# Optimization experiments

Hardware: AMD Instinct MI355X
Metric: run time of the kernel (lower is better)

Reference implementation:

```python
import jax, jax.numpy as jnp
import numpy as np
from jax import lax

B, T, D, NL, NH, FF, NC, SMAX, MAXS = 4, 160000, 768, 12, 12, 2048, 100, 64, 200
CONV_SPEC = [(512, 10, 5), (512, 3, 2), (512, 3, 2), (512, 3, 2), (512, 2, 2), (512, 2, 2), (768, 2, 2)]
TP = 499  # frames after conv stack for T=160000


def _ln(x, w, b, eps=1e-5):
    m = x.mean(-1, keepdims=True)
    v = ((x - m) ** 2).mean(-1, keepdims=True)
    return (x - m) * lax.rsqrt(v + eps) * w + b


def setup_inputs() -> dict:
    key = jax.random.key(0)
    ks = iter(jax.random.split(key, 64))
    d = {}
    d['x'] = jax.random.normal(next(ks), (B, 1, T), jnp.float32)
    d['seg_bounds'] = jnp.sort(jax.random.randint(next(ks), (B, SMAX + 1), 0, TP), axis=-1)
    d['n_segs'] = jax.random.randint(next(ks), (B,), SMAX // 2, SMAX + 1)
    in_c = 1
    for i, (oc, k, s) in enumerate(CONV_SPEC):
        d[f'conv_w{i}'] = jax.random.normal(next(ks), (oc, in_c, k), jnp.float32) * 0.02
        d[f'conv_b{i}'] = jnp.zeros((oc,), jnp.float32)
        in_c = oc
    d['attn_v'] = jax.random.normal(next(ks), (D,), jnp.float32)  # torch.randn init
    d['pos_emb'] = jax.random.normal(next(ks), (MAXS, D), jnp.float32) * 0.02
    d['in_w'] = jax.random.normal(next(ks), (NL, 3 * D, D), jnp.float32) * 0.02
    d['in_b'] = jnp.zeros((NL, 3 * D), jnp.float32)
    d['out_w'] = jax.random.normal(next(ks), (NL, D, D), jnp.float32) * 0.02
    d['out_b'] = jnp.zeros((NL, D), jnp.float32)
    d['ff1_w'] = jax.random.normal(next(ks), (NL, FF, D), jnp.float32) * 0.02
    d['ff1_b'] = jnp.zeros((NL, FF), jnp.float32)
    d['ff2_w'] = jax.random.normal(next(ks), (NL, D, FF), jnp.float32) * 0.02
    d['ff2_b'] = jnp.zeros((NL, D), jnp.float32)
    d['ln1_w'] = jnp.ones((NL, D), jnp.float32)
    d['ln1_b'] = jnp.zeros((NL, D), jnp.float32)
    d['ln2_w'] = jnp.ones((NL, D), jnp.float32)
    d['ln2_b'] = jnp.zeros((NL, D), jnp.float32)
    d['fln_w'] = jnp.ones((D,), jnp.float32)
    d['fln_b'] = jnp.zeros((D,), jnp.float32)
    d['proj_w'] = jax.random.normal(next(ks), (NC, D), jnp.float32) * 0.02
    d['proj_b'] = jnp.zeros((NC,), jnp.float32)
    return d


def reference(x, seg_bounds, n_segs,
              conv_w0, conv_b0, conv_w1, conv_b1, conv_w2, conv_b2, conv_w3, conv_b3,
              conv_w4, conv_b4, conv_w5, conv_b5, conv_w6, conv_b6,
              attn_v, pos_emb, in_w, in_b, out_w, out_b,
              ff1_w, ff1_b, ff2_w, ff2_b, ln1_w, ln1_b, ln2_w, ln2_b,
              fln_w, fln_b, proj_w, proj_b):
    # ---- conv feature extractor (Conv1d + ReLU stack), NCW layout ----
    ws = [conv_w0, conv_w1, conv_w2, conv_w3, conv_w4, conv_w5, conv_w6]
    bs = [conv_b0, conv_b1, conv_b2, conv_b3, conv_b4, conv_b5, conv_b6]
    h = x
    for w, b, (_, _, s) in zip(ws, bs, CONV_SPEC):
        h = lax.conv_general_dilated(h, w, (s,), 'VALID',
                                     dimension_numbers=('NCH', 'OIH', 'NCH'))
        h = jax.nn.relu(h + b[None, :, None])
    feats = h.transpose(0, 2, 1)  # [B, Tp, D]
    Tp = feats.shape[1]

    # ---- vectorized per-segment attention pooling (replaces ragged python loop) ----
    starts = jnp.clip(seg_bounds[:, :-1], 0, Tp - 1)           # [B, Smax]
    ends = jnp.maximum(starts + 1, jnp.clip(seg_bounds[:, 1:], 0, Tp))
    pad_mask = jnp.arange(SMAX)[None, :] >= n_segs[:, None]    # [B, Smax] True=pad
    t = jnp.arange(Tp)
    fm = (t[None, None, :] >= starts[..., None]) & (t[None, None, :] < ends[..., None]) \
         & (~pad_mask[..., None])                              # [B, Smax, Tp]
    scores = jnp.einsum('btc,c->bt', feats, attn_v)[:, None, :]  # [B, 1, Tp]
    m = jnp.max(jnp.where(fm, scores, -jnp.inf), axis=-1, keepdims=True)
    m = jnp.where(jnp.isfinite(m), m, 0.0)
    e = jnp.where(fm, jnp.exp(scores - m), 0.0)
    den = e.sum(-1, keepdims=True)
    wgt = e / jnp.where(den > 0, den, 1.0)                     # masked softmax over frames
    tokens = jnp.einsum('bst,btc->bsc', wgt, feats)            # [B, Smax, D]; pads are zeros

    tokens = tokens + pos_emb[:SMAX][None]

    # ---- post-norm transformer encoder (torch TransformerEncoderLayer defaults) ----
    dh = D // NH
    scale = 1.0 / np.sqrt(dh)

    def layer(tok, p):
        iw, ib, ow, ob, f1w, f1b, f2w, f2b, l1w, l1b, l2w, l2b = p
        qkv = tok @ iw.T + ib
        q, k, v = jnp.split(qkv, 3, axis=-1)
        def heads(z):
            return z.reshape(B, SMAX, NH, dh).transpose(0, 2, 1, 3)
        q, k, v = heads(q), heads(k), heads(v)
        att = jnp.einsum('bhqd,bhkd->bhqk', q, k) * scale
        att = jnp.where(pad_mask[:, None, None, :], -1e9, att)  # key padding mask
        att = jax.nn.softmax(att, axis=-1)
        o = jnp.einsum('bhqk,bhkd->bhqd', att, v).transpose(0, 2, 1, 3).reshape(B, SMAX, D)
        o = o @ ow.T + ob
        tok = _ln(tok + o, l1w, l1b)
        f = jax.nn.relu(tok @ f1w.T + f1b) @ f2w.T + f2b
        tok = _ln(tok + f, l2w, l2b)
        return tok, None

    tokens, _ = lax.scan(layer, tokens,
                         (in_w, in_b, out_w, out_b, ff1_w, ff1_b, ff2_w, ff2_b,
                          ln1_w, ln1_b, ln2_w, ln2_b))

    y = _ln(tokens, fln_w, fln_b)
    logits = y @ proj_w.T + proj_b
    return logits, pad_mask
```

## Files before the change

kernel.cpp:

```cpp
#include <hip/hip_runtime.h>
#include <hip/hip_bf16.h>

#define BATCH 4
#define TIN0 160000
#define DMODEL 768
#define NLAYER 12
#define FFDIM 2048
#define NCLS 100
#define SMAX_ 64
#define TP_ 499

typedef __attribute__((ext_vector_type(8))) short short8;
typedef __attribute__((ext_vector_type(4))) float f32x4;

__device__ inline ushort f2b(float f) { __hip_bfloat16 h = __float2bfloat16(f); return *(ushort*)&h; }
__device__ inline float b2f(ushort u) { __hip_bfloat16 h = *(__hip_bfloat16*)&u; return __bfloat162float(h); }

__device__ inline void gl_lds16(const ushort* g, ushort* l) {
    __builtin_amdgcn_global_load_lds((const __attribute__((address_space(1))) unsigned int*)g,
                                     (__attribute__((address_space(3))) unsigned int*)l, 16, 0, 0);
}

__device__ inline float wave_reduce_sum(float v) {
#pragma unroll
    for (int off = 32; off > 0; off >>= 1) v += __shfl_down(v, off, 64);
    return v;
}
__device__ inline float wave_reduce_max(float v) {
#pragma unroll
    for (int off = 32; off > 0; off >>= 1) v = fmaxf(v, __shfl_down(v, off, 64));
    return v;
}
__device__ inline float block_reduce_sum(float v, float* scratch) {
    v = wave_reduce_sum(v);
    int wid = threadIdx.x >> 6;
    if ((threadIdx.x & 63) == 0) scratch[wid] = v;
    __syncthreads();
    float r = scratch[0] + scratch[1] + scratch[2] + scratch[3];
    __syncthreads();
    return r;
}
__device__ inline float block_reduce_max(float v, float* scratch) {
    v = wave_reduce_max(v);
    int wid = threadIdx.x >> 6;
    if ((threadIdx.x & 63) == 0) scratch[wid] = v;
    __syncthreads();
    float r = fmaxf(fmaxf(scratch[0], scratch[1]), fmaxf(scratch[2], scratch[3]));
    __syncthreads();
    return r;
}

template <int KW, int STRIDE, int RELU, int OBF, int BF32>
__global__ __launch_bounds__(256) void conv_mfma(
    const ushort* __restrict__ A,
    const ushort* __restrict__ Wc,
    const float* __restrict__ Wf,
    const float* __restrict__ bias,
    void* __restrict__ outv,
    int Cin, int Cout, int Tout, int tBase, int uBase,
    long aStride, long oStride) {
    const int K = KW * Cin;
    const int nCh = K >> 5;
    const int CPK = Cin >> 5;
    const int t0 = tBase + blockIdx.x * 128;
    const int oc0 = blockIdx.y * 128;
    const int b = blockIdx.z;
    const ushort* Ab = A + (size_t)b * aStride;

    __shared__ ushort sA[4096];
    __shared__ ushort sB[4096];

    const int tid = threadIdx.x;
    const int lane = tid & 63;
    const int wv = tid >> 6;
    const int rsub = lane >> 2;
    const int kgW = (lane & 3) ^ ((lane >> 3) & 3);
    const int mrow = lane & 15;
    const int kq = lane >> 4;
    const int slot8 = (mrow * 4 + (kq ^ ((mrow >> 1) & 3))) * 8;

    f32x4 acc[2][8];
#pragma unroll
    for (int s = 0; s < 2; s++)
#pragma unroll
        for (int n = 0; n < 8; n++) acc[s][n] = (f32x4){0.f, 0.f, 0.f, 0.f};

    for (int c = 0; c < nCh; c++) {
        const int kw = (KW == 1) ? 0 : (c / CPK);
        const int icc = (c - kw * CPK) << 5;
#pragma unroll
        for (int j = 0; j < 2; j++) {
            int t = t0 + j * 64 + wv * 16 + rsub;
            if (t > Tout - 1) t = Tout - 1;
            int u = STRIDE * t + kw - uBase;
            gl_lds16(Ab + (size_t)u * Cin + icc + kgW * 8, &sA[(j * 64 + wv * 16) * 32]);
        }
#pragma unroll
        for (int j = 0; j < 2; j++) {
            int rowb = oc0 + j * 64 + wv * 16 + rsub;
            if (rowb > Cout - 1) rowb = Cout - 1;
            if (BF32) {
                const float* wp = Wf + (size_t)rowb * K + c * 32 + kgW * 8;
                float4 w0_ = *(const float4*)wp;
                float4 w1_ = *(const float4*)(wp + 4);
                short8 vals;
                vals[0] = (short)f2b(w0_.x); vals[1] = (short)f2b(w0_.y);
                vals[2] = (short)f2b(w0_.z); vals[3] = (short)f2b(w0_.w);
                vals[4] = (short)f2b(w1_.x); vals[5] = (short)f2b(w1_.y);
                vals[6] = (short)f2b(w1_.z); vals[7] = (short)f2b(w1_.w);
                *(short8*)&sB[(j * 64 + wv * 16) * 32 + lane * 8] = vals;
            } else {
                gl_lds16(Wc + (size_t)rowb * K + c * 32 + kgW * 8, &sB[(j * 64 + wv * 16) * 32]);
            }
        }
        __syncthreads();
        short8 a0 = *(const short8*)&sA[(wv * 32 + 0) * 32 + slot8];
        short8 a1 = *(const short8*)&sA[(wv * 32 + 16) * 32 + slot8];
#pragma unroll
        for (int n = 0; n < 8; n++) {
            short8 bf = *(const short8*)&sB[(n * 16) * 32 + slot8];
            acc[0][n] = __builtin_amdgcn_mfma_f32_16x16x32_bf16(a0, bf, acc[0][n], 0, 0, 0);
            acc[1][n] = __builtin_amdgcn_mfma_f32_16x16x32_bf16(a1, bf, acc[1][n], 0, 0, 0);
        }
        __syncthreads();
    }

    float* outf = (float*)outv + (size_t)b * oStride;
    ushort* outh = (ushort*)outv + (size_t)b * oStride;
    float bz[8];
#pragma unroll
    for (int n = 0; n < 8; n++) {
        int oc = oc0 + n * 16 + mrow;
        bz[n] = (oc < Cout) ? bias[oc] : 0.f;
    }
#pragma unroll
    for (int s = 0; s < 2; s++) {
        int tb = t0 + wv * 32 + s * 16 + kq * 4;
#pragma unroll
        for (int n = 0; n < 8; n++) {
            int oc = oc0 + n * 16 + mrow;
            if (oc >= Cout) continue;
#pragma unroll
            for (int r = 0; r < 4; r++) {
                int t = tb + r;
                if (t < Tout) {
                    float v = acc[s][n][r] + bz[n];
                    if (RELU) v = fmaxf(v, 0.f);
                    if (OBF) outh[(size_t)t * Cout + oc] = f2b(v);
                    else outf[(size_t)t * Cout + oc] = v;
                }
            }
        }
    }
}

__global__ __launch_bounds__(256) void gemm_sk(
    const ushort* __restrict__ A, const float* __restrict__ Wf,
    const float* __restrict__ bias, float* __restrict__ outp,
    int M, int K, int KCH, long oSlab) {
    __shared__ ushort sA[4096];
    __shared__ ushort sB[4096];
    const int tid = threadIdx.x;
    const int lane = tid & 63;
    const int wv = tid >> 6;
    const int rsub = lane >> 2;
    const int kgW = (lane & 3) ^ ((lane >> 3) & 3);
    const int mrow = lane & 15;
    const int kq = lane >> 4;
    const int slot8 = (mrow * 4 + (kq ^ ((mrow >> 1) & 3))) * 8;
    const int t0 = blockIdx.x * 128;
    const int oc0 = blockIdx.y * 128;
    const int kc = blockIdx.z;
    const int k0 = kc * KCH;

    f32x4 acc[2][8];
#pragma unroll
    for (int s = 0; s < 2; s++)
#pragma unroll
        for (int n = 0; n < 8; n++) acc[s][n] = (f32x4){0.f, 0.f, 0.f, 0.f};

    const int nIt = KCH >> 5;
    for (int c = 0; c < nIt; c++) {
        const int kk = k0 + (c << 5);
#pragma unroll
        for (int j = 0; j < 2; j++) {
            int t = t0 + j * 64 + wv * 16 + rsub;
            gl_lds16(A + (size_t)t * K + kk + kgW * 8, &sA[(j * 64 + wv * 16) * 32]);
        }
#pragma unroll
        for (int j = 0; j < 2; j++) {
            int rowb = oc0 + j * 64 + wv * 16 + rsub;
            const float* wp = Wf + (size_t)rowb * K + kk + kgW * 8;
            float4 w0_ = *(const float4*)wp;
            float4 w1_ = *(const float4*)(wp + 4);
            short8 vals;
            vals[0] = (short)f2b(w0_.x); vals[1] = (short)f2b(w0_.y);
            vals[2] = (short)f2b(w0_.z); vals[3] = (short)f2b(w0_.w);
            vals[4] = (short)f2b(w1_.x); vals[5] = (short)f2b(w1_.y);
            vals[6] = (short)f2b(w1_.z); vals[7] = (short)f2b(w1_.w);
            *(short8*)&sB[(j * 64 + wv * 16) * 32 + lane * 8] = vals;
        }
        __syncthreads();
        short8 a0 = *(const short8*)&sA[(wv * 32 + 0) * 32 + slot8];
        short8 a1 = *(const short8*)&sA[(wv * 32 + 16) * 32 + slot8];
#pragma unroll
        for (int n = 0; n < 8; n++) {
            short8 bf = *(const short8*)&sB[(n * 16) * 32 + slot8];
            acc[0][n] = __builtin_amdgcn_mfma_f32_16x16x32_bf16(a0, bf, acc[0][n], 0, 0, 0);
            acc[1][n] = __builtin_amdgcn_mfma_f32_16x16x32_bf16(a1, bf, acc[1][n], 0, 0, 0);
        }
        __syncthreads();
    }

    float* op = outp + (size_t)kc * oSlab;
#pragma unroll
    for (int s = 0; s < 2; s++) {
        int tb = t0 + wv * 32 + s * 16 + kq * 4;
#pragma unroll
        for (int n = 0; n < 8; n++) {
            int oc = oc0 + n * 16 + mrow;
            float bz = (kc == 0) ? bias[oc] : 0.f;
#pragma unroll
            for (int r = 0; r < 4; r++) {
                op[(size_t)(tb + r) * M + oc] = acc[s][n][r] + bz;
            }
        }
    }
}

__global__ __launch_bounds__(256) void relu_cast(const float* __restrict__ p,
                                                 ushort* __restrict__ o,
                                                 long n, long slab) {
    for (long i = (long)blockIdx.x * 1024 + threadIdx.x; i < n; i += (long)gridDim.x * 1024) {
#pragma unroll
        for (int j = 0; j < 4; j++) {
            long k = i + (long)j * 256;
            if (k < n) {
                float v = p[k] + p[k + slab] + p[k + 2 * slab];
                o[k] = f2b(fmaxf(v, 0.f));
            }
        }
    }
}

__global__ __launch_bounds__(256) void conv0_mfma(const float* __restrict__ x,
                                                  const ushort* __restrict__ w0pad,
                                                  const float* __restrict__ b0,
                                                  ushort* __restrict__ c0,
                                                  int uBase, int nU) {
    __shared__ ushort sA[4096];
    __shared__ ushort sB[4096];
    const int tid = threadIdx.x;
    const int lane = tid & 63;
    const int wv = tid >> 6;
    const int rsub = lane >> 2;
    const int kgW = (lane & 3) ^ ((lane >> 3) & 3);
    const int mrow = lane & 15;
    const int kq = lane >> 4;
    const int slot8 = (mrow * 4 + (kq ^ ((mrow >> 1) & 3))) * 8;
    const int r0 = blockIdx.x * 128;
    const int oc0 = blockIdx.y * 128;

    f32x4 acc[2][8];
#pragma unroll
    for (int s = 0; s < 2; s++)
#pragma unroll
        for (int n = 0; n < 8; n++) acc[s][n] = (f32x4){0.f, 0.f, 0.f, 0.f};

#pragma unroll
    for (int j = 0; j < 2; j++) {
        int r = r0 + j * 64 + wv * 16 + rsub;
        if (r > nU - 1) r = nU - 1;
        const float* xp = x + (size_t)5 * (uBase + r);
        short8 vals = (short8){0, 0, 0, 0, 0, 0, 0, 0};
        if (kgW == 0) {
#pragma unroll
            for (int q = 0; q < 8; q++) vals[q] = (short)f2b(xp[q]);
        } else if (kgW == 1) {
            vals[0] = (short)f2b(xp[8]);
            vals[1] = (short)f2b(xp[9]);
        }
        *(short8*)&sA[(j * 64 + wv * 16) * 32 + lane * 8] = vals;
    }
#pragma unroll
    for (int j = 0; j < 2; j++) {
        int rowb = oc0 + j * 64 + wv * 16 + rsub;
        gl_lds16(w0pad + (size_t)rowb * 32 + kgW * 8, &sB[(j * 64 + wv * 16) * 32]);
    }
    __syncthreads();
    short8 a0 = *(const short8*)&sA[(wv * 32 + 0) * 32 + slot8];
    short8 a1 = *(const short8*)&sA[(wv * 32 + 16) * 32 + slot8];
#pragma unroll
    for (int n = 0; n < 8; n++) {
        short8 bf = *(const short8*)&sB[(n * 16) * 32 + slot8];
        acc[0][n] = __builtin_amdgcn_mfma_f32_16x16x32_bf16(a0, bf, acc[0][n], 0, 0, 0);
        acc[1][n] = __builtin_amdgcn_mfma_f32_16x16x32_bf16(a1, bf, acc[1][n], 0, 0, 0);
    }
#pragma unroll
    for (int s = 0; s < 2; s++) {
        int rb = r0 + wv * 32 + s * 16 + kq * 4;
#pragma unroll
        for (int n = 0; n < 8; n++) {
            int oc = oc0 + n * 16 + mrow;
            float bz = b0[oc];
#pragma unroll
            for (int r = 0; r < 4; r++) {
                int rr = rb + r;
                if (rr < nU) c0[(size_t)rr * 512 + oc] = f2b(fmaxf(acc[s][n][r] + bz, 0.f));
            }
        }
    }
}

__global__ __launch_bounds__(256) void convw_kernel(
    const float* __restrict__ w1, const float* __restrict__ w2, const float* __restrict__ w3,
    const float* __restrict__ w4, const float* __restrict__ w5, const float* __restrict__ w6,
    const float* __restrict__ w0, ushort* __restrict__ dst, ushort* __restrict__ dw0) {
    const int z = blockIdx.y;
    const int COUTS[6] = {512, 512, 512, 512, 512, 768};
    const int KWS[6] = {3, 3, 3, 2, 2, 2};
    const long OFFS[6] = {0, 786432, 1572864, 2359296, 2883584, 3407872};
    const float* srcs[6] = {w1, w2, w3, w4, w5, w6};
    if (z == 6) {
        for (int o = blockIdx.x * 256 + threadIdx.x; o < 512 * 32; o += gridDim.x * 256) {
            int oc = o >> 5, q = o & 31;
            dw0[o] = (q < 10) ? f2b(w0[oc * 10 + q]) : (ushort)0;
        }
        return;
    }
    const float* src = srcs[z];
    ushort* d = dst + OFFS[z];
    const int Cin = 512, Kw = KWS[z];
    const int K = Cin * Kw;
    const long n = (long)COUTS[z] * K;
    for (long o = blockIdx.x * 256 + threadIdx.x; o < n; o += (long)gridDim.x * 256) {
        long oc = o / K;
        int rem = (int)(o - oc * K);
        int kw = rem / Cin, ic = rem - kw * Cin;
        d[o] = f2b(src[(oc * Cin + ic) * Kw + kw]);
    }
}

__global__ __launch_bounds__(256) void scores_kernel(const ushort* __restrict__ feats,
                                                     const float* __restrict__ v,
                                                     float* __restrict__ scores) {
    int b = blockIdx.y;
    int t = blockIdx.x * 4 + (threadIdx.x >> 6);
    if (t >= TP_) return;
    int lane = threadIdx.x & 63;
    const ushort* f = feats + ((size_t)b * TP_ + t) * DMODEL + lane * 12;
    float acc = 0.f;
#pragma unroll
    for (int q = 0; q < 12; q++) acc = fmaf(b2f(f[q]), v[lane * 12 + q], acc);
    acc = wave_reduce_sum(acc);
    if (lane == 0) scores[b * TP_ + t] = acc;
}

__global__ __launch_bounds__(256) void pool_kernel(const ushort* __restrict__ featsAll,
                                                   const float* __restrict__ scoresAll,
                                                   const int* __restrict__ seg_bounds,
                                                   const int* __restrict__ n_segs,
                                                   const float* __restrict__ pos_emb,
                                                   float* __restrict__ tokens,
                                                   ushort* __restrict__ tokens_bf) {
    __shared__ float scratch[4];
    __shared__ float wgt[512];
    int s = blockIdx.x, b = blockIdx.y, tid = threadIdx.x;
    float* tout = tokens + ((size_t)b * SMAX_ + s) * DMODEL;
    ushort* tbf = tokens_bf + ((size_t)b * SMAX_ + s) * DMODEL;
    int ns = n_segs[b];
    if (s >= ns) {
        for (int c = tid; c < DMODEL; c += 256) {
            float v = pos_emb[s * DMODEL + c];
            tout[c] = v; tbf[c] = f2b(v);
        }
        return;
    }
    const float* sc = scoresAll + b * TP_;
    int b0 = seg_bounds[b * (SMAX_ + 1) + s];
    int b1 = seg_bounds[b * (SMAX_ + 1) + s + 1];
    int st = min(max(b0, 0), TP_ - 1);
    int en = max(st + 1, min(max(b1, 0), TP_));
    float lm = -1e30f;
    for (int t = st + tid; t < en; t += 256) lm = fmaxf(lm, sc[t]);
    float m = block_reduce_max(lm, scratch);
    float ls = 0.f;
    for (int t = st + tid; t < en; t += 256) ls += __expf(sc[t] - m);
    float den = block_reduce_sum(ls, scratch);
    float inv = 1.f / den;
    for (int t = st + tid; t < en; t += 256) wgt[t - st] = __expf(sc[t] - m) * inv;
    __syncthreads();
    int len = en - st;
    const ushort* f = featsAll + ((size_t)b * TP_ + st) * DMODEL;
    float a0 = 0.f, a1 = 0.f, a2 = 0.f;
    for (int t = 0; t < len; t++) {
        float wv = wgt[t];
        const ushort* fr = f + (size_t)t * DMODEL;
        a0 = fmaf(wv, b2f(fr[tid]), a0);
        a1 = fmaf(wv, b2f(fr[tid + 256]), a1);
        a2 = fmaf(wv, b2f(fr[tid + 512]), a2);
    }
    float v0 = a0 + pos_emb[s * DMODEL + tid];
    float v1 = a1 + pos_emb[s * DMODEL + tid + 256];
    float v2 = a2 + pos_emb[s * DMODEL + tid + 512];
    tout[tid] = v0; tout[tid + 256] = v1; tout[tid + 512] = v2;
    tbf[tid] = f2b(v0); tbf[tid + 256] = f2b(v1); tbf[tid + 512] = f2b(v2);
}

__global__ __launch_bounds__(256) void attn_kernel(const float* __restrict__ qkv_p,
                                                   const int* __restrict__ n_segs,
                                                   ushort* __restrict__ o, long slab) {
    __shared__ float sK[64][68];
    __shared__ float sV[64][68];
    __shared__ float sS[64][68];
    int h = blockIdx.x, b = blockIdx.y, tid = threadIdx.x;
    int ns = n_segs[b];
    const float* base = qkv_p + (size_t)b * 64 * 2304 + h * 64;
    for (int idx = tid; idx < 4096; idx += 256) {
        int s_ = idx >> 6, d = idx & 63;
        size_t kofs = (size_t)s_ * 2304 + 768 + d;
        size_t vofs = (size_t)s_ * 2304 + 1536 + d;
        sK[s_][d] = base[kofs] + base[kofs + slab] + base[kofs + 2 * slab];
        sV[s_][d] = base[vofs] + base[vofs + slab] + base[vofs + 2 * slab];
    }
    __syncthreads();
    int qr = tid >> 2;
    int c0 = (tid & 3) * 16;
    const float* qrow = base + (size_t)qr * 2304;
    float acc[16];
#pragma unroll
    for (int j = 0; j < 16; j++) acc[j] = 0.f;
    for (int d = 0; d < 64; d += 4) {
        float4 q0 = *(const float4*)(qrow + d);
        float4 q1 = *(const float4*)(qrow + slab + d);
        float4 q2 = *(const float4*)(qrow + 2 * slab + d);
        float4 qv = make_float4(q0.x + q1.x + q2.x, q0.y + q1.y + q2.y,
                                q0.z + q1.z + q2.z, q0.w + q1.w + q2.w);
#pragma unroll
        for (int j = 0; j < 16; j++) {
            float4 kv = *(const float4*)&sK[c0 + j][d];
            acc[j] += qv.x * kv.x + qv.y * kv.y + qv.z * kv.z + qv.w * kv.w;
        }
    }
#pragma unroll
    for (int j = 0; j < 16; j++) {
        int kc = c0 + j;
        float vv = acc[j] * 0.125f;
        if (kc >= ns) vv = -1e9f;
        sS[qr][kc] = vv;
    }
    __syncthreads();
    if (tid < 64) {
        float m = -1e30f;
#pragma unroll 4
        for (int k = 0; k < 64; k++) m = fmaxf(m, sS[tid][k]);
        float ssum = 0.f;
#pragma unroll 4
        for (int k = 0; k < 64; k++) {
            float e = __expf(sS[tid][k] - m);
            sS[tid][k] = e;
            ssum += e;
        }
        float inv = 1.f / ssum;
#pragma unroll 4
        for (int k = 0; k < 64; k++) sS[tid][k] *= inv;
    }
    __syncthreads();
    float4 oacc[4];
#pragma unroll
    for (int j = 0; j < 4; j++) oacc[j] = make_float4(0.f, 0.f, 0.f, 0.f);
    for (int k = 0; k < 64; k++) {
        float wv = sS[qr][k];
#pragma unroll
        for (int j4 = 0; j4 < 4; j4++) {
            float4 vv = *(const float4*)&sV[k][c0 + j4 * 4];
            oacc[j4].x = fmaf(wv, vv.x, oacc[j4].x);
            oacc[j4].y = fmaf(wv, vv.y, oacc[j4].y);
            oacc[j4].z = fmaf(wv, vv.z, oacc[j4].z);
            oacc[j4].w = fmaf(wv, vv.w, oacc[j4].w);
        }
    }
    ushort* orow = o + ((size_t)b * 64 + qr) * DMODEL + h * 64 + c0;
#pragma unroll
    for (int j4 = 0; j4 < 4; j4++) {
        orow[j4 * 4 + 0] = f2b(oacc[j4].x);
        orow[j4 * 4 + 1] = f2b(oacc[j4].y);
        orow[j4 * 4 + 2] = f2b(oacc[j4].z);
        orow[j4 * 4 + 3] = f2b(oacc[j4].w);
    }
}

__global__ __launch_bounds__(256) void ln_kernel(const float* __restrict__ x,
                                                 const float* __restrict__ rP, int nP, long rSlab,
                                                 const float* __restrict__ w,
                                                 const float* __restrict__ b,
                                                 float* __restrict__ out,
                                                 ushort* __restrict__ outbf) {
    __shared__ float scratch[4];
    int row = blockIdx.x, tid = threadIdx.x;
    const float* xr = x + (size_t)row * DMODEL;
    float v0 = xr[tid], v1 = xr[tid + 256], v2 = xr[tid + 512];
    for (int p = 0; p < nP; p++) {
        const float* rr = rP + (size_t)p * rSlab + (size_t)row * DMODEL;
        v0 += rr[tid]; v1 += rr[tid + 256]; v2 += rr[tid + 512];
    }
    float mean = block_reduce_sum(v0 + v1 + v2, scratch) * (1.f / DMODEL);
    float d0 = v0 - mean, d1 = v1 - mean, d2 = v2 - mean;
    float var = block_reduce_sum(d0 * d0 + d1 * d1 + d2 * d2, scratch) * (1.f / DMODEL);
    float inv = rsqrtf(var + 1e-5f);
    float o0 = d0 * inv * w[tid] + b[tid];
    float o1 = d1 * inv * w[tid + 256] + b[tid + 256];
    float o2 = d2 * inv * w[tid + 512] + b[tid + 512];
    float* orow = out + (size_t)row * DMODEL;
    orow[tid] = o0; orow[tid + 256] = o1; orow[tid + 512] = o2;
    if (outbf) {
        ushort* obf = outbf + (size_t)row * DMODEL;
        obf[tid] = f2b(o0); obf[tid + 256] = f2b(o1); obf[tid + 512] = f2b(o2);
    }
}

__global__ void mask_kernel(const int* __restrict__ n_segs, float* __restrict__ mout) {
    int i = threadIdx.x;
    int b = i >> 6, s = i & 63;
    mout[i] = (s >= n_segs[b]) ? 1.0f : 0.0f;
}

extern "C" void kernel_launch(void* const* d_in, const int* in_sizes, int n_in,
                              void* d_out, int out_size, void* d_ws, size_t ws_size,
                              hipStream_t stream) {
    const float* x = (const float*)d_in[0];
    const int* seg_bounds = (const int*)d_in[1];
    const int* n_segs = (const int*)d_in[2];
    const float* cw[7], * cb[7];
    for (int i = 0; i < 7; i++) { cw[i] = (const float*)d_in[3 + 2 * i]; cb[i] = (const float*)d_in[4 + 2 * i]; }
    const float* attn_v = (const float*)d_in[17];
    const float* pos_emb = (const float*)d_in[18];
    const float* in_w = (const float*)d_in[19];
    const float* in_b = (const float*)d_in[20];
    const float* out_w = (const float*)d_in[21];
    const float* out_b = (const float*)d_in[22];
    const float* ff1_w = (const float*)d_in[23];
    const float* ff1_b = (const float*)d_in[24];
    const float* ff2_w = (const float*)d_in[25];
    const float* ff2_b = (const float*)d_in[26];
    const float* ln1_w = (const float*)d_in[27];
    const float* ln1_b = (const float*)d_in[28];
    const float* ln2_w = (const float*)d_in[29];
    const float* ln2_b = (const float*)d_in[30];
    const float* fln_w = (const float*)d_in[31];
    const float* fln_b = (const float*)d_in[32];
    const float* proj_w = (const float*)d_in[33];
    const float* proj_b = (const float*)d_in[34];

    mask_kernel<<<1, 256, 0, stream>>>(n_segs, (float*)d_out + 256 * NCLS);

    size_t off = 0;
    auto alloc = [&](size_t bytes) {
        void* p = (char*)d_ws + off;
        off += (bytes + 255) & ~(size_t)255;
        return p;
    };
    ushort* wbc = (ushort*)alloc(4194304ULL * 2);
    ushort* w0pad = (ushort*)alloc(512ULL * 32 * 2);
    ushort* c0buf = (ushort*)alloc((size_t)16001 * 512 * 2);
    ushort* out1 = (ushort*)alloc((size_t)15999 * 512 * 2);
    ushort* out4 = (ushort*)alloc((size_t)4 * 1999 * 512 * 2);
    float* scores = (float*)alloc((size_t)4 * TP_ * 4);
    float* tokens = (float*)alloc((size_t)256 * DMODEL * 4);
    ushort* tokens_bf = (ushort*)alloc((size_t)256 * DMODEL * 2);
    ushort* oall_bf = (ushort*)alloc((size_t)256 * DMODEL * 2);
    float* ybuf = (float*)alloc((size_t)256 * DMODEL * 4);
    ushort* ybf = (ushort*)alloc((size_t)256 * DMODEL * 2);
    if (off > ws_size) return;

    ushort* out2b = c0buf;
    ushort* out3b = out1 + (size_t)12000 * 512;
    ushort* out5 = c0buf;
    ushort* feats = out1;
    float* qkv_p = (float*)c0buf;
    float* ffh_p = (float*)c0buf + (size_t)3 * 256 * 2304;
    ushort* ffh_bf = (ushort*)(ffh_p + (size_t)3 * 256 * 2048);
    float* tmp_p = (float*)out4;

    ushort* wc1 = wbc, * wc2 = wbc + 786432, * wc3 = wbc + 1572864,
          * wc4 = wbc + 2359296, * wc5 = wbc + 2883584, * wc6 = wbc + 3407872;

    convw_kernel<<<dim3(512, 7), 256, 0, stream>>>(cw[1], cw[2], cw[3], cw[4], cw[5], cw[6],
                                                   cw[0], wbc, w0pad);

    for (int b = 0; b < BATCH; b++) {
        const float* xb = x + (size_t)b * TIN0;
        conv0_mfma<<<dim3(126, 4), 256, 0, stream>>>(xb, w0pad, cb[0], c0buf, 0, 16001);
        conv_mfma<3, 2, 1, 1, 0><<<dim3(63, 4, 1), 256, 0, stream>>>(
            c0buf, wc1, nullptr, cb[1], out1, 512, 512, 8000, 0, 0, 0, 0);
        conv0_mfma<<<dim3(125, 4), 256, 0, stream>>>(xb, w0pad, cb[0], c0buf, 16000, 15999);
        conv_mfma<3, 2, 1, 1, 0><<<dim3(63, 4, 1), 256, 0, stream>>>(
            c0buf, wc1, nullptr, cb[1], out1, 512, 512, 15999, 8000, 16000, 0, 0);
        conv_mfma<3, 2, 1, 1, 0><<<dim3(63, 4, 1), 256, 0, stream>>>(
            out1, wc2, nullptr, cb[2], out2b, 512, 512, 7999, 0, 0, 0, 0);
        conv_mfma<3, 2, 1, 1, 0><<<dim3(32, 4, 1), 256, 0, stream>>>(
            out2b, wc3, nullptr, cb[3], out3b, 512, 512, 3999, 0, 0, 0, 0);
        conv_mfma<2, 2, 1, 1, 0><<<dim3(16, 4, 1), 256, 0, stream>>>(
            out3b, wc4, nullptr, cb[4], out4 + (size_t)b * 1999 * 512,
            512, 512, 1999, 0, 0, 0, 0);
    }
    conv_mfma<2, 2, 1, 1, 0><<<dim3(8, 4, BATCH), 256, 0, stream>>>(
        out4, wc5, nullptr, cb[5], out5, 512, 512, 999, 0, 0,
        (long)1999 * 512, (long)999 * 512);
    conv_mfma<2, 2, 1, 1, 0><<<dim3(4, 6, BATCH), 256, 0, stream>>>(
        out5, wc6, nullptr, cb[6], feats, 512, 768, 499, 0, 0,
        (long)999 * 512, (long)499 * 768);

    scores_kernel<<<dim3(125, 4), 256, 0, stream>>>(feats, attn_v, scores);
    pool_kernel<<<dim3(SMAX_, 4), 256, 0, stream>>>(feats, scores, seg_bounds, n_segs,
                                                    pos_emb, tokens, tokens_bf);

    const long qkvSlab = (long)256 * 2304;
    const long tmpSlab = (long)256 * 768;
    const long ffhSlab = (long)256 * 2048;
    for (int l = 0; l < NLAYER; l++) {
        const float* iw = in_w + (size_t)l * 2304 * DMODEL;
        const float* ib = in_b + (size_t)l * 2304;
        const float* ow = out_w + (size_t)l * DMODEL * DMODEL;
        const float* ob = out_b + (size_t)l * DMODEL;
        const float* f1w = ff1_w + (size_t)l * FFDIM * DMODEL;
        const float* f1b = ff1_b + (size_t)l * FFDIM;
        const float* f2w = ff2_w + (size_t)l * DMODEL * FFDIM;
        const float* f2b_ = ff2_b + (size_t)l * DMODEL;

        gemm_sk<<<dim3(2, 18, 3), 256, 0, stream>>>(tokens_bf, iw, ib, qkv_p, 2304, 768, 256, qkvSlab);
        attn_kernel<<<dim3(12, 4), 256, 0, stream>>>(qkv_p, n_segs, oall_bf, qkvSlab);
        gemm_sk<<<dim3(2, 6, 3), 256, 0, stream>>>(oall_bf, ow, ob, tmp_p, 768, 768, 256, tmpSlab);
        ln_kernel<<<256, 256, 0, stream>>>(tokens, tmp_p, 3, tmpSlab,
                                           ln1_w + l * DMODEL, ln1_b + l * DMODEL, tokens, tokens_bf);
        gemm_sk<<<dim3(2, 16, 3), 256, 0, stream>>>(tokens_bf, f1w, f1b, ffh_p, 2048, 768, 256, ffhSlab);
        relu_cast<<<512, 256, 0, stream>>>(ffh_p, ffh_bf, (long)256 * 2048, ffhSlab);
        gemm_sk<<<dim3(2, 6, 4), 256, 0, stream>>>(ffh_bf, f2w, f2b_, tmp_p, 768, 2048, 512, tmpSlab);
        ln_kernel<<<256, 256, 0, stream>>>(tokens, tmp_p, 4, tmpSlab,
                                           ln2_w + l * DMODEL, ln2_b + l * DMODEL, tokens, tokens_bf);
    }

    ln_kernel<<<256, 256, 0, stream>>>(tokens, nullptr, 0, 0, fln_w, fln_b, ybuf, ybf);
    conv_mfma<1, 1, 0, 0, 1><<<dim3(2, 1, 1), 256, 0, stream>>>(
        ybf, nullptr, proj_w, proj_b, (float*)d_out, 768, NCLS, 256, 0, 0, 0, 0);
}
```

Baseline: 2.648 ms.

## Add input-reusing strided conv kernel and raise split-K depth in transformer GEMMs

```diff
diff --git a/kernel.cpp b/kernel.cpp
--- a/kernel.cpp
+++ b/kernel.cpp
@@ -48,6 +48,107 @@
     float r = fmaxf(fmaxf(scratch[0], scratch[1]), fmaxf(scratch[2], scratch[3]));
     __syncthreads();
     return r;
+}
+
+template <int KW>
+__global__ __launch_bounds__(256) void convT_mfma(
+    const ushort* __restrict__ A,
+    const ushort* __restrict__ Wc,
+    const float* __restrict__ bias,
+    ushort* __restrict__ outp,
+    int Cin, int Cout, int Tout,
+    int tBase, int uBase, int uMax,
+    long aStride, long oStride) {
+    constexpr int EB = 132;
+    __shared__ ushort sA[288 * 64];
+    __shared__ ushort sB[KW * 128 * 32];
+    const int tid = threadIdx.x;
+    const int lane = tid & 63;
+    const int wv = tid >> 6;
+    const int mrow = lane & 15;
+    const int kq = lane >> 4;
+    const int t0 = tBase + blockIdx.x * 128;
+    const int oc0 = blockIdx.y * 128;
+    const ushort* Ab = A + (size_t)blockIdx.z * aStride;
+    ushort* outb = outp + (size_t)blockIdx.z * oStride;
+    const int K = KW * Cin;
+
+    f32x4 acc[2][8];
+#pragma unroll
+    for (int s = 0; s < 2; s++)
+#pragma unroll
+        for (int n = 0; n < 8; n++) acc[s][n] = (f32x4){0.f, 0.f, 0.f, 0.f};
+
+    const int nC8 = Cin >> 6;
+    for (int c8 = 0; c8 < nC8; c8++) {
+        const int ic0 = c8 << 6;
+#pragma unroll
+        for (int rd = 0; rd < 9; rd++) {
+            int slotBase = rd * 256 + wv * 64;
+            int slot = slotBase + lane;
+            int r = slot >> 3;
+            int g = (slot & 7) ^ (r & 7);
+            int u = (r < EB) ? (2 * t0 + 2 * r) : (2 * t0 + 2 * (r - EB) + 1);
+            u -= uBase;
+            if (u < 0) u = 0;
+            if (u > uMax) u = uMax;
+            gl_lds16(Ab + (size_t)u * Cin + ic0 + g * 8, &sA[slotBase * 8]);
+        }
+#pragma unroll
+        for (int h = 0; h < 2; h++) {
+#pragma unroll
+            for (int rd = 0; rd < KW * 2; rd++) {
+                int slotBase = rd * 256 + wv * 64;
+                int slot = slotBase + lane;
+                int r = slot >> 2;
+                int g = (slot & 3) ^ ((r >> 1) & 3);
+                int ocr = oc0 + (r & 127);
+                if (ocr > Cout - 1) ocr = Cout - 1;
+                int kwi = r >> 7;
+                gl_lds16(Wc + (size_t)ocr * K + kwi * Cin + ic0 + h * 32 + g * 8,
+                         &sB[slotBase * 8]);
+            }
+            __syncthreads();
+#pragma unroll
+            for (int kw = 0; kw < KW; kw++) {
+                const int abase = (kw & 1) ? EB : 0;
+                const int aoff = kw >> 1;
+#pragma unroll
+                for (int s = 0; s < 2; s++) {
+                    int ar = abase + wv * 32 + s * 16 + mrow + aoff;
+                    short8 af = *(const short8*)&sA[ar * 64 + (((h * 4 + kq) ^ (ar & 7)) * 8)];
+#pragma unroll
+                    for (int n = 0; n < 8; n++) {
+                        int br = kw * 128 + n * 16 + mrow;
+                        short8 bf = *(const short8*)&sB[br * 32 + ((kq ^ ((br >> 1) & 3)) * 8)];
+                        acc[s][n] = __builtin_amdgcn_mfma_f32_16x16x32_bf16(af, bf, acc[s][n], 0, 0, 0);
+                    }
+                }
+            }
+            __syncthreads();
+        }
+    }
+
+    float bz[8];
+#pragma unroll
+    for (int n = 0; n < 8; n++) {
+        int oc = oc0 + n * 16 + mrow;
+        bz[n] = (oc < Cout) ? bias[oc] : 0.f;
+    }
+#pragma unroll
+    for (int s = 0; s < 2; s++) {
+        int tb = t0 + wv * 32 + s * 16 + kq * 4;
+#pragma unroll
+        for (int n = 0; n < 8; n++) {
+            int oc = oc0 + n * 16 + mrow;
+            if (oc >= Cout) continue;
+#pragma unroll
+            for (int r = 0; r < 4; r++) {
+                int t = tb + r;
+                if (t < Tout) outb[(size_t)t * Cout + oc] = f2b(fmaxf(acc[s][n][r] + bz[n], 0.f));
+            }
+        }
+    }
 }
 
 template <int KW, int STRIDE, int RELU, int OBF, int BF32>
@@ -61,15 +162,12 @@
     long aStride, long oStride) {
     const int K = KW * Cin;
     const int nCh = K >> 5;
-    const int CPK = Cin >> 5;
     const int t0 = tBase + blockIdx.x * 128;
     const int oc0 = blockIdx.y * 128;
     const int b = blockIdx.z;
     const ushort* Ab = A + (size_t)b * aStride;
-
     __shared__ ushort sA[4096];
     __shared__ ushort sB[4096];
-
     const int tid = threadIdx.x;
     const int lane = tid & 63;
     const int wv = tid >> 6;
@@ -86,14 +184,12 @@
         for (int n = 0; n < 8; n++) acc[s][n] = (f32x4){0.f, 0.f, 0.f, 0.f};
 
     for (int c = 0; c < nCh; c++) {
-        const int kw = (KW == 1) ? 0 : (c / CPK);
-        const int icc = (c - kw * CPK) << 5;
 #pragma unroll
         for (int j = 0; j < 2; j++) {
             int t = t0 + j * 64 + wv * 16 + rsub;
             if (t > Tout - 1) t = Tout - 1;
-            int u = STRIDE * t + kw - uBase;
-            gl_lds16(Ab + (size_t)u * Cin + icc + kgW * 8, &sA[(j * 64 + wv * 16) * 32]);
+            int u = STRIDE * t - uBase;
+            gl_lds16(Ab + (size_t)u * Cin + c * 32 + kgW * 8, &sA[(j * 64 + wv * 16) * 32]);
         }
 #pragma unroll
         for (int j = 0; j < 2; j++) {
@@ -124,7 +220,6 @@
         }
         __syncthreads();
     }
-
     float* outf = (float*)outv + (size_t)b * oStride;
     ushort* outh = (ushort*)outv + (size_t)b * oStride;
     float bz[8];
@@ -230,13 +325,14 @@
 
 __global__ __launch_bounds__(256) void relu_cast(const float* __restrict__ p,
                                                  ushort* __restrict__ o,
-                                                 long n, long slab) {
+                                                 long n, long slab, int nP) {
     for (long i = (long)blockIdx.x * 1024 + threadIdx.x; i < n; i += (long)gridDim.x * 1024) {
 #pragma unroll
         for (int j = 0; j < 4; j++) {
             long k = i + (long)j * 256;
             if (k < n) {
-                float v = p[k] + p[k + slab] + p[k + 2 * slab];
+                float v = 0.f;
+                for (int q = 0; q < nP; q++) v += p[k + q * slab];
                 o[k] = f2b(fmaxf(v, 0.f));
             }
         }
@@ -409,7 +505,7 @@
 
 __global__ __launch_bounds__(256) void attn_kernel(const float* __restrict__ qkv_p,
                                                    const int* __restrict__ n_segs,
-                                                   ushort* __restrict__ o, long slab) {
+                                                   ushort* __restrict__ o, long slab, int nP) {
     __shared__ float sK[64][68];
     __shared__ float sV[64][68];
     __shared__ float sS[64][68];
@@ -420,8 +516,9 @@
         int s_ = idx >> 6, d = idx & 63;
         size_t kofs = (size_t)s_ * 2304 + 768 + d;
         size_t vofs = (size_t)s_ * 2304 + 1536 + d;
-        sK[s_][d] = base[kofs] + base[kofs + slab] + base[kofs + 2 * slab];
-        sV[s_][d] = base[vofs] + base[vofs + slab] + base[vofs + 2 * slab];
+        float kv = 0.f, vv = 0.f;
+        for (int p = 0; p < nP; p++) { kv += base[kofs + p * slab]; vv += base[vofs + p * slab]; }
+        sK[s_][d] = kv; sV[s_][d] = vv;
     }
     __syncthreads();
     int qr = tid >> 2;
@@ -431,11 +528,11 @@
 #pragma unroll
     for (int j = 0; j < 16; j++) acc[j] = 0.f;
     for (int d = 0; d < 64; d += 4) {
-        float4 q0 = *(const float4*)(qrow + d);
-        float4 q1 = *(const float4*)(qrow + slab + d);
-        float4 q2 = *(const float4*)(qrow + 2 * slab + d);
-        float4 qv = make_float4(q0.x + q1.x + q2.x, q0.y + q1.y + q2.y,
-                                q0.z + q1.z + q2.z, q0.w + q1.w + q2.w);
+        float4 qv = make_float4(0.f, 0.f, 0.f, 0.f);
+        for (int p = 0; p < nP; p++) {
+            float4 qp = *(const float4*)(qrow + p * slab + d);
+            qv.x += qp.x; qv.y += qp.y; qv.z += qp.z; qv.w += qp.w;
+        }
 #pragma unroll
         for (int j = 0; j < 16; j++) {
             float4 kv = *(const float4*)&sK[c0 + j][d];
@@ -578,9 +675,9 @@
     ushort* out5 = c0buf;
     ushort* feats = out1;
     float* qkv_p = (float*)c0buf;
-    float* ffh_p = (float*)c0buf + (size_t)3 * 256 * 2304;
-    ushort* ffh_bf = (ushort*)(ffh_p + (size_t)3 * 256 * 2048);
-    float* tmp_p = (float*)out4;
+    float* ffh_p = (float*)c0buf + (size_t)4 * 256 * 2304;
+    ushort* ffh_bf = (ushort*)out4;
+    float* tmp_p = (float*)((char*)out4 + (size_t)256 * 2048 * 2);
 
     ushort* wc1 = wbc, * wc2 = wbc + 786432, * wc3 = wbc + 1572864,
           * wc4 = wbc + 2359296, * wc5 = wbc + 2883584, * wc6 = wbc + 3407872;
@@ -591,24 +688,23 @@
     for (int b = 0; b < BATCH; b++) {
         const float* xb = x + (size_t)b * TIN0;
         conv0_mfma<<<dim3(126, 4), 256, 0, stream>>>(xb, w0pad, cb[0], c0buf, 0, 16001);
-        conv_mfma<3, 2, 1, 1, 0><<<dim3(63, 4, 1), 256, 0, stream>>>(
-            c0buf, wc1, nullptr, cb[1], out1, 512, 512, 8000, 0, 0, 0, 0);
+        convT_mfma<3><<<dim3(63, 4, 1), 256, 0, stream>>>(
+            c0buf, wc1, cb[1], out1, 512, 512, 15999, 0, 0, 16000, 0, 0);
         conv0_mfma<<<dim3(125, 4), 256, 0, stream>>>(xb, w0pad, cb[0], c0buf, 16000, 15999);
-        conv_mfma<3, 2, 1, 1, 0><<<dim3(63, 4, 1), 256, 0, stream>>>(
-            c0buf, wc1, nullptr, cb[1], out1, 512, 512, 15999, 8000, 16000, 0, 0);
-        conv_mfma<3, 2, 1, 1, 0><<<dim3(63, 4, 1), 256, 0, stream>>>(
-            out1, wc2, nullptr, cb[2], out2b, 512, 512, 7999, 0, 0, 0, 0);
-        conv_mfma<3, 2, 1, 1, 0><<<dim3(32, 4, 1), 256, 0, stream>>>(
-            out2b, wc3, nullptr, cb[3], out3b, 512, 512, 3999, 0, 0, 0, 0);
-        conv_mfma<2, 2, 1, 1, 0><<<dim3(16, 4, 1), 256, 0, stream>>>(
-            out3b, wc4, nullptr, cb[4], out4 + (size_t)b * 1999 * 512,
-            512, 512, 1999, 0, 0, 0, 0);
-    }
-    conv_mfma<2, 2, 1, 1, 0><<<dim3(8, 4, BATCH), 256, 0, stream>>>(
-        out4, wc5, nullptr, cb[5], out5, 512, 512, 999, 0, 0,
+        convT_mfma<3><<<dim3(63, 4, 1), 256, 0, stream>>>(
+            c0buf, wc1, cb[1], out1, 512, 512, 15999, 8000, 16000, 15998, 0, 0);
+        convT_mfma<3><<<dim3(63, 4, 1), 256, 0, stream>>>(
+            out1, wc2, cb[2], out2b, 512, 512, 7999, 0, 0, 15998, 0, 0);
+        convT_mfma<3><<<dim3(32, 4, 1), 256, 0, stream>>>(
+            out2b, wc3, cb[3], out3b, 512, 512, 3999, 0, 0, 7998, 0, 0);
+        convT_mfma<2><<<dim3(16, 4, 1), 256, 0, stream>>>(
+            out3b, wc4, cb[4], out4 + (size_t)b * 1999 * 512, 512, 512, 1999, 0, 0, 3998, 0, 0);
+    }
+    convT_mfma<2><<<dim3(8, 4, BATCH), 256, 0, stream>>>(
+        out4, wc5, cb[5], out5, 512, 512, 999, 0, 0, 1998,
         (long)1999 * 512, (long)999 * 512);
-    conv_mfma<2, 2, 1, 1, 0><<<dim3(4, 6, BATCH), 256, 0, stream>>>(
-        out5, wc6, nullptr, cb[6], feats, 512, 768, 499, 0, 0,
+    convT_mfma<2><<<dim3(4, 6, BATCH), 256, 0, stream>>>(
+        out5, wc6, cb[6], feats, 512, 768, 499, 0, 0, 998,
         (long)999 * 512, (long)499 * 768);
 
     scores_kernel<<<dim3(125, 4), 256, 0, stream>>>(feats, attn_v, scores);
@@ -628,15 +724,15 @@
         const float* f2w = ff2_w + (size_t)l * DMODEL * FFDIM;
         const float* f2b_ = ff2_b + (size_t)l * DMODEL;
 
-        gemm_sk<<<dim3(2, 18, 3), 256, 0, stream>>>(tokens_bf, iw, ib, qkv_p, 2304, 768, 256, qkvSlab);
-        attn_kernel<<<dim3(12, 4), 256, 0, stream>>>(qkv_p, n_segs, oall_bf, qkvSlab);
-        gemm_sk<<<dim3(2, 6, 3), 256, 0, stream>>>(oall_bf, ow, ob, tmp_p, 768, 768, 256, tmpSlab);
-        ln_kernel<<<256, 256, 0, stream>>>(tokens, tmp_p, 3, tmpSlab,
+        gemm_sk<<<dim3(2, 18, 4), 256, 0, stream>>>(tokens_bf, iw, ib, qkv_p, 2304, 768, 192, qkvSlab);
+        attn_kernel<<<dim3(12, 4), 256, 0, stream>>>(qkv_p, n_segs, oall_bf, qkvSlab, 4);
+        gemm_sk<<<dim3(2, 6, 4), 256, 0, stream>>>(oall_bf, ow, ob, tmp_p, 768, 768, 192, tmpSlab);
+        ln_kernel<<<256, 256, 0, stream>>>(tokens, tmp_p, 4, tmpSlab,
                                            ln1_w + l * DMODEL, ln1_b + l * DMODEL, tokens, tokens_bf);
         gemm_sk<<<dim3(2, 16, 3), 256, 0, stream>>>(tokens_bf, f1w, f1b, ffh_p, 2048, 768, 256, ffhSlab);
-        relu_cast<<<512, 256, 0, stream>>>(ffh_p, ffh_bf, (long)256 * 2048, ffhSlab);
-        gemm_sk<<<dim3(2, 6, 4), 256, 0, stream>>>(ffh_bf, f2w, f2b_, tmp_p, 768, 2048, 512, tmpSlab);
-        ln_kernel<<<256, 256, 0, stream>>>(tokens, tmp_p, 4, tmpSlab,
+        relu_cast<<<512, 256, 0, stream>>>(ffh_p, ffh_bf, (long)256 * 2048, ffhSlab, 3);
+        gemm_sk<<<dim3(2, 6, 8), 256, 0, stream>>>(ffh_bf, f2w, f2b_, tmp_p, 768, 2048, 256, tmpSlab);
+        ln_kernel<<<256, 256, 0, stream>>>(tokens, tmp_p, 8, tmpSlab,
                                            ln2_w + l * DMODEL, ln2_b + l * DMODEL, tokens, tokens_bf);
     }
 
```

After: 2.555 ms. 3.5% less time.
